# Kernel optimization log

Hardware: AMD Instinct MI355X
Metric: run time of the kernel (lower is better)

## Reference

```python
import jax, jax.numpy as jnp
import numpy as np

DIM = 32
HID = 128          # edge-MLP hidden width
N = 8192           # total nodes
E = 131072         # total edges
B = 64             # number of graphs
NUM_MP = 3
S2S_STEPS = 3


def setup_inputs() -> dict:
    key = jax.random.key(0)
    ks = jax.random.split(key, 24)
    g = lambda k, shape, s=0.05: jax.random.normal(k, shape, dtype=jnp.float32) * s

    inp = {
        "x": jax.random.normal(ks[0], (N, 1), dtype=jnp.float32),
        "edge_attr": jax.random.uniform(ks[1], (E, 2), dtype=jnp.float32),
        # params
        "lin0_w": g(ks[2], (1, DIM)), "lin0_b": g(ks[3], (DIM,)),
        "enn_w1": g(ks[4], (2, HID)), "enn_b1": g(ks[5], (HID,)),
        "enn_w2": g(ks[6], (HID, DIM * DIM)), "enn_b2": g(ks[7], (DIM * DIM,)),
        "root_w": g(ks[8], (DIM, DIM)), "conv_b": g(ks[9], (DIM,)),
        # GRU (gates ordered r,z,n as in torch)
        "gru_wih": g(ks[10], (DIM, 3 * DIM)), "gru_whh": g(ks[11], (DIM, 3 * DIM)),
        "gru_bih": g(ks[12], (3 * DIM,)), "gru_bhh": g(ks[13], (3 * DIM,)),
        # Set2Set LSTM: input 2*DIM, hidden DIM (gates ordered i,f,g,o as in torch)
        "s2s_wih": g(ks[14], (2 * DIM, 4 * DIM)), "s2s_whh": g(ks[15], (DIM, 4 * DIM)),
        "s2s_bih": g(ks[16], (4 * DIM,)), "s2s_bhh": g(ks[17], (4 * DIM,)),
        "lin1_w": g(ks[18], (2 * DIM, DIM)), "lin1_b": g(ks[19], (DIM,)),
        "lin2_w": g(ks[20], (DIM, 1)), "lin2_b": g(ks[21], (1,)),
        # int args
        "edge_index": jax.random.randint(ks[22], (2, E), 0, N, dtype=jnp.int32),
        "batch": jnp.sort(jax.random.randint(ks[23], (N,), 0, B, dtype=jnp.int32)),
    }
    return inp


def _forward(x, edge_attr, lin0_w, lin0_b, enn_w1, enn_b1, enn_w2, enn_b2,
             root_w, conv_b, gru_wih, gru_whh, gru_bih, gru_bhh,
             s2s_wih, s2s_whh, s2s_bih, s2s_bhh, lin1_w, lin1_b, lin2_w, lin2_b,
             edge_index, batch):
    src, dst = edge_index[0], edge_index[1]

    out = jax.nn.relu(x @ lin0_w + lin0_b)          # [N, DIM]
    h = out                                          # GRU hidden state

    # edge-conditioned weights (constant across MP layers -> hoisted)
    ew = jax.nn.relu(edge_attr @ enn_w1 + enn_b1) @ enn_w2 + enn_b2
    W = ew.reshape(E, DIM, DIM)                      # [E, in, out]

    deg = jnp.maximum(jax.ops.segment_sum(jnp.ones((E,), jnp.float32), dst,
                                          num_segments=N), 1.0)[:, None]

    for _ in range(NUM_MP):
        # NNConv: gather -> per-edge small matmul -> scatter-mean, + root + bias
        msg = jnp.einsum('ed,edo->eo', out[src], W)  # [E, DIM]
        agg = jax.ops.segment_sum(msg, dst, num_segments=N) / deg
        m = jax.nn.relu(agg + out @ root_w + conv_b)
        # GRU cell (single step)
        gi = m @ gru_wih + gru_bih
        gh = h @ gru_whh + gru_bhh
        ir, iz, in_ = jnp.split(gi, 3, axis=-1)
        hr, hz, hn = jnp.split(gh, 3, axis=-1)
        r = jax.nn.sigmoid(ir + hr)
        z = jax.nn.sigmoid(iz + hz)
        n = jnp.tanh(in_ + r * hn)
        h = (1.0 - z) * n + z * h
        out = h

    # Set2Set pooling
    qh = jnp.zeros((B, DIM), jnp.float32)
    qc = jnp.zeros((B, DIM), jnp.float32)
    q_star = jnp.zeros((B, 2 * DIM), jnp.float32)
    for _ in range(S2S_STEPS):
        gates = q_star @ s2s_wih + s2s_bih + qh @ s2s_whh + s2s_bhh
        i_, f_, g_, o_ = jnp.split(gates, 4, axis=-1)
        qc = jax.nn.sigmoid(f_) * qc + jax.nn.sigmoid(i_) * jnp.tanh(g_)
        qh = jax.nn.sigmoid(o_) * jnp.tanh(qc)       # [B, DIM]
        e = jnp.sum(out * qh[batch], axis=-1)        # [N] attention logits
        emax = jax.ops.segment_max(e, batch, num_segments=B)
        a = jnp.exp(e - emax[batch])
        a = a / jax.ops.segment_sum(a, batch, num_segments=B)[batch]
        r_read = jax.ops.segment_sum(a[:, None] * out, batch, num_segments=B)
        q_star = jnp.concatenate([qh, r_read], axis=-1)  # [B, 2*DIM]

    y = jax.nn.relu(q_star @ lin1_w + lin1_b) @ lin2_w + lin2_b
    return y.reshape(-1)                              # [B]


def reference(x, edge_attr, lin0_w, lin0_b, enn_w1, enn_b1, enn_w2, enn_b2,
              root_w, conv_b, gru_wih, gru_whh, gru_bih, gru_bhh,
              s2s_wih, s2s_whh, s2s_bih, s2s_bhh, lin1_w, lin1_b, lin2_w, lin2_b,
              edge_index, batch):
    return _forward(x, edge_attr, lin0_w, lin0_b, enn_w1, enn_b1, enn_w2, enn_b2,
                    root_w, conv_b, gru_wih, gru_whh, gru_bih, gru_bhh,
                    s2s_wih, s2s_whh, s2s_bih, s2s_bhh, lin1_w, lin1_b, lin2_w,
                    lin2_b, edge_index, batch)
```

## Files before the change

kernel.cpp:

```cpp
#include <hip/hip_runtime.h>

#define N_NODES 8192
#define N_EDGES 131072
#define NGRAPH  64
#define DIM     32
#define HID     128
#define KHALF   64
#define G_NODES 3
#define SROW    34

__device__ __forceinline__ float sigmoidf_(float x) { return 1.0f / (1.0f + expf(-x)); }

__global__ void prep1_kernel(const float* __restrict__ x, const float* __restrict__ w,
                             const float* __restrict__ b, float* __restrict__ out,
                             const int* __restrict__ dst, int* __restrict__ counts) {
  const int bb = blockIdx.x;
  if (bb < 1024) {
    int idx = bb * 256 + threadIdx.x;
    int n = idx >> 5, d = idx & 31;
    out[idx] = fmaxf(fmaf(x[n], w[d], b[d]), 0.0f);
  } else {
    int e = (bb - 1024) * 256 + threadIdx.x;
    atomicAdd(&counts[dst[e]], 1);
  }
}

__global__ void scan_kernel(const int* __restrict__ counts,
                            int* __restrict__ offsets,
                            float* __restrict__ deg_inv) {
  __shared__ int sm[1024];
  int t = threadIdx.x;
  int base = t * 8;
  int loc[8];
  int s = 0;
#pragma unroll
  for (int i = 0; i < 8; ++i) { loc[i] = s; s += counts[base + i]; }
  sm[t] = s;
  __syncthreads();
  for (int off = 1; off < 1024; off <<= 1) {
    int v = (t >= off) ? sm[t - off] : 0;
    __syncthreads();
    sm[t] += v;
    __syncthreads();
  }
  int excl = (t > 0) ? sm[t - 1] : 0;
#pragma unroll
  for (int i = 0; i < 8; ++i) {
    offsets[base + i] = excl + loc[i];
    int c = counts[base + i];
    deg_inv[base + i] = 1.0f / (float)(c > 0 ? c : 1);
  }
  if (t == 1023) offsets[N_NODES] = sm[1023];
}

__global__ void prep2_kernel(const int* __restrict__ ei, const float* __restrict__ ea,
                             const int* __restrict__ offsets, int* __restrict__ cursor,
                             int* __restrict__ csr_src, float2* __restrict__ csr_ea,
                             const int* __restrict__ batch, int* __restrict__ gstart) {
  const int bb = blockIdx.x;
  if (bb < 512) {
    int e = bb * 256 + threadIdx.x;
    int d = ei[N_EDGES + e];
    int pos = atomicAdd(&cursor[d], 1);
    int slot = offsets[d] + pos;
    csr_src[slot] = ei[e];
    csr_ea[slot] = make_float2(ea[2 * e], ea[2 * e + 1]);
  } else {
    int n = (bb - 512) * 256 + threadIdx.x;
    int b = batch[n];
    if (n == 0) {
      for (int g = 0; g <= b; ++g) gstart[g] = 0;
    } else {
      int bp = batch[n - 1];
      for (int g = bp + 1; g <= b; ++g) gstart[g] = n;
    }
    if (n == N_NODES - 1) {
      for (int g = b + 1; g <= NGRAPH; ++g) gstart[g] = N_NODES;
    }
  }
}

__global__ __launch_bounds__(256, 4) void mp_half_kernel(
    const float* __restrict__ out_cur, const int* __restrict__ offsets,
    const int* __restrict__ csr_src, const float2* __restrict__ csr_ea,
    const float* __restrict__ w1, const float* __restrict__ b1,
    const float* __restrict__ w2, float* __restrict__ partial,
    float* __restrict__ O) {
  constexpr int C = 16;
  __shared__ float smem[G_NODES * KHALF * SROW + C * KHALF + C * DIM];
  float* S = smem;
  float* hidb = smem + G_NODES * KHALF * SROW;
  float* osrcb = hidb + C * KHALF;
  float* red = smem;
  __shared__ int offs[G_NODES + 1];

  const int t = threadIdx.x;
  const int bb = blockIdx.x;
  const int khalf = bb & 1;
  const int node0 = (bb >> 1) * G_NODES;

  if (t <= G_NODES) offs[t] = offsets[min(node0 + t, N_NODES)];

  const int kg = t >> 4, dg = t & 15;
  const int k0 = kg * 4, d0 = dg * 2;
  const int ec = t >> 4, sub = t & 15;

  float acc[G_NODES][4][2];
#pragma unroll
  for (int g = 0; g < G_NODES; ++g)
#pragma unroll
    for (int i = 0; i < 4; ++i) { acc[g][i][0] = 0.0f; acc[g][i][1] = 0.0f; }
  float oacc[G_NODES] = {0.0f, 0.0f, 0.0f};
  __syncthreads();

#pragma unroll
  for (int g = 0; g < G_NODES; ++g) {
    const int base = offs[g], end = offs[g + 1];
    for (int c0 = base; c0 < end; c0 += C) {
      const int cnt = min(C, end - c0);
      __syncthreads();
      if (ec < cnt) {
        const int slot = c0 + ec;
        const float2 eav = csr_ea[slot];
        const int sidx = csr_src[slot];
#pragma unroll
        for (int i = 0; i < 4; ++i) {
          const int kl = sub * 4 + i;
          const int kgl = khalf * KHALF + kl;
          hidb[ec * KHALF + kl] =
              fmaxf(fmaf(eav.y, w1[HID + kgl], fmaf(eav.x, w1[kgl], b1[kgl])), 0.0f);
        }
        *(float2*)(osrcb + ec * DIM + sub * 2) =
            *(const float2*)(out_cur + sidx * DIM + sub * 2);
      }
      __syncthreads();
      for (int e = 0; e < cnt; ++e) {
        const float4 hv = *(const float4*)(hidb + e * KHALF + k0);
        const float2 ov = *(const float2*)(osrcb + e * DIM + d0);
        acc[g][0][0] = fmaf(hv.x, ov.x, acc[g][0][0]);
        acc[g][0][1] = fmaf(hv.x, ov.y, acc[g][0][1]);
        acc[g][1][0] = fmaf(hv.y, ov.x, acc[g][1][0]);
        acc[g][1][1] = fmaf(hv.y, ov.y, acc[g][1][1]);
        acc[g][2][0] = fmaf(hv.z, ov.x, acc[g][2][0]);
        acc[g][2][1] = fmaf(hv.z, ov.y, acc[g][2][1]);
        acc[g][3][0] = fmaf(hv.w, ov.x, acc[g][3][0]);
        acc[g][3][1] = fmaf(hv.w, ov.y, acc[g][3][1]);
        if (khalf == 0 && t < DIM) oacc[g] += osrcb[e * DIM + t];
      }
    }
  }
#pragma unroll
  for (int g = 0; g < G_NODES; ++g) {
    float* Sg = S + g * KHALF * SROW;
#pragma unroll
    for (int i = 0; i < 4; ++i)
      *(float2*)(Sg + (k0 + i) * SROW + d0) = make_float2(acc[g][i][0], acc[g][i][1]);
  }
  if (khalf == 0 && t < DIM) {
#pragma unroll
    for (int g = 0; g < G_NODES; ++g) {
      const int node = node0 + g;
      if (node < N_NODES) O[node * DIM + t] = oacc[g];
    }
  }
  __syncthreads();

  {
    const int ks = t >> 4;
    const int dvh = (t >> 3) & 1;
    const int og = t & 7;
    float a4[G_NODES][4];
#pragma unroll
    for (int g = 0; g < G_NODES; ++g)
#pragma unroll
      for (int r = 0; r < 4; ++r) a4[g][r] = 0.0f;
#pragma unroll
    for (int i = 0; i < 4; ++i) {
      const int kl = ks * 4 + i;
      const float* w2k = w2 + (size_t)(khalf * KHALF + kl) * (DIM * DIM);
#pragma unroll
      for (int dvi = 0; dvi < 4; ++dvi) {
        const int dv = dvh * 4 + dvi;
#pragma unroll
        for (int r = 0; r < 4; ++r) {
          const int d = dv * 4 + r;
          const float4 wv = *(const float4*)(w2k + d * DIM + og * 4);
#pragma unroll
          for (int g = 0; g < G_NODES; ++g) {
            const float sv = S[g * KHALF * SROW + kl * SROW + d];
            a4[g][0] = fmaf(sv, wv.x, a4[g][0]);
            a4[g][1] = fmaf(sv, wv.y, a4[g][1]);
            a4[g][2] = fmaf(sv, wv.z, a4[g][2]);
            a4[g][3] = fmaf(sv, wv.w, a4[g][3]);
          }
        }
      }
    }
    __syncthreads();
#pragma unroll
    for (int g = 0; g < G_NODES; ++g)
#pragma unroll
      for (int r = 0; r < 4; ++r) red[(g * 4 + r) * 256 + t] = a4[g][r];
  }
  __syncthreads();
  if (t < G_NODES * DIM) {
    const int g = t >> 5, o = t & 31;
    const int og = o >> 2, r = o & 3;
    const float* rp = red + (g * 4 + r) * 256 + og;
    float sum = 0.0f;
#pragma unroll
    for (int j = 0; j < 32; ++j) sum += rp[j * 8];
    const int node = node0 + g;
    if (node < N_NODES)
      partial[(size_t)khalf * N_NODES * DIM + node * DIM + o] = sum;
  }
}

__global__ __launch_bounds__(256) void epilogue_kernel(
    const float* __restrict__ partial, const float* __restrict__ O,
    const float* __restrict__ out_cur, const float* __restrict__ b2,
    const float* __restrict__ deg_inv, const float* __restrict__ root_w,
    const float* __restrict__ conv_b, const float* __restrict__ gwih,
    const float* __restrict__ gwhh, const float* __restrict__ gbih,
    const float* __restrict__ gbhh, float* __restrict__ out_nxt) {
  __shared__ float hb[256], ob[256], mb[256], b2s[1024];
  const int t = threadIdx.x;
  const int node0 = blockIdx.x * 8;
  hb[t] = out_cur[node0 * DIM + t];
  ob[t] = O[node0 * DIM + t];
#pragma unroll
  for (int i = 0; i < 4; ++i) b2s[i * 256 + t] = b2[i * 256 + t];
  __syncthreads();
  const int g = t >> 5, o = t & 31;
  const int node = node0 + g;
  float agg = partial[node * DIM + o] +
              partial[(size_t)N_NODES * DIM + node * DIM + o];
#pragma unroll
  for (int d = 0; d < DIM; ++d) agg = fmaf(ob[g * DIM + d], b2s[d * DIM + o], agg);
  agg *= deg_inv[node];
  float rt = conv_b[o];
#pragma unroll
  for (int d = 0; d < DIM; ++d) rt = fmaf(hb[g * DIM + d], root_w[d * DIM + o], rt);
  mb[t] = fmaxf(agg + rt, 0.0f);
  __syncthreads();
  float gi[3], gh[3];
#pragma unroll
  for (int jj = 0; jj < 3; ++jj) {
    float si = gbih[jj * DIM + o], sh = gbhh[jj * DIM + o];
#pragma unroll
    for (int d = 0; d < DIM; ++d) {
      si = fmaf(mb[g * DIM + d], gwih[d * 3 * DIM + jj * DIM + o], si);
      sh = fmaf(hb[g * DIM + d], gwhh[d * 3 * DIM + jj * DIM + o], sh);
    }
    gi[jj] = si;
    gh[jj] = sh;
  }
  const float r = sigmoidf_(gi[0] + gh[0]);
  const float z = sigmoidf_(gi[1] + gh[1]);
  const float nn = tanhf(fmaf(r, gh[2], gi[2]));
  out_nxt[node * DIM + o] = (1.0f - z) * nn + z * hb[t];
}

__global__ __launch_bounds__(256) void s2s_kernel(
    const float* __restrict__ outf, const int* __restrict__ gstart,
    const float* __restrict__ wih, const float* __restrict__ whh,
    const float* __restrict__ bih, const float* __restrict__ bhh,
    const float* __restrict__ l1w, const float* __restrict__ l1b,
    const float* __restrict__ l2w, const float* __restrict__ l2b,
    float* __restrict__ y) {
  __shared__ float qh[DIM], qc[DIM], qstar[2 * DIM], gates[4 * DIM];
  __shared__ float wsum[4], wmax[4], wr[4][DIM];
  const int b = blockIdx.x, t = threadIdx.x;
  const int gs = gstart[b], ge = gstart[b + 1];
  const int w = t >> 6, lane = t & 63;
  if (t < DIM) { qh[t] = 0.0f; qc[t] = 0.0f; }
  if (t < 2 * DIM) qstar[t] = 0.0f;
  __syncthreads();
  for (int step = 0; step < 3; ++step) {
    if (t < 4 * DIM) {
      float gv = bih[t] + bhh[t];
      for (int i = 0; i < 2 * DIM; ++i) gv = fmaf(qstar[i], wih[i * 4 * DIM + t], gv);
      for (int i = 0; i < DIM; ++i) gv = fmaf(qh[i], whh[i * 4 * DIM + t], gv);
      gates[t] = gv;
    }
    __syncthreads();
    if (t < DIM) {
      const float ig = sigmoidf_(gates[t]);
      const float fg = sigmoidf_(gates[DIM + t]);
      const float gg = tanhf(gates[2 * DIM + t]);
      const float og = sigmoidf_(gates[3 * DIM + t]);
      const float c = fmaf(fg, qc[t], ig * gg);
      qc[t] = c;
      qh[t] = og * tanhf(c);
    }
    __syncthreads();
    float lmax = -INFINITY;
    for (int n = gs + t; n < ge; n += 256) {
      const float* orow = outf + n * DIM;
      float e = 0.0f;
#pragma unroll
      for (int d = 0; d < DIM; ++d) e = fmaf(orow[d], qh[d], e);
      lmax = fmaxf(lmax, e);
    }
#pragma unroll
    for (int off = 32; off > 0; off >>= 1) lmax = fmaxf(lmax, __shfl_xor(lmax, off));
    if (lane == 0) wmax[w] = lmax;
    __syncthreads();
    const float gmax = fmaxf(fmaxf(wmax[0], wmax[1]), fmaxf(wmax[2], wmax[3]));
    float rl[DIM];
#pragma unroll
    for (int d = 0; d < DIM; ++d) rl[d] = 0.0f;
    float lsum = 0.0f;
    for (int n = gs + t; n < ge; n += 256) {
      const float* orow = outf + n * DIM;
      float e = 0.0f;
#pragma unroll
      for (int d = 0; d < DIM; ++d) e = fmaf(orow[d], qh[d], e);
      const float a = expf(e - gmax);
      lsum += a;
#pragma unroll
      for (int d = 0; d < DIM; ++d) rl[d] = fmaf(a, orow[d], rl[d]);
    }
#pragma unroll
    for (int off = 32; off > 0; off >>= 1) {
      lsum += __shfl_xor(lsum, off);
#pragma unroll
      for (int d = 0; d < DIM; ++d) rl[d] += __shfl_xor(rl[d], off);
    }
    __syncthreads();
    if (lane == 0) {
      wsum[w] = lsum;
#pragma unroll
      for (int d = 0; d < DIM; ++d) wr[w][d] = rl[d];
    }
    __syncthreads();
    if (t < DIM) {
      const float stot = wsum[0] + wsum[1] + wsum[2] + wsum[3];
      const float rv = wr[0][t] + wr[1][t] + wr[2][t] + wr[3][t];
      qstar[t] = qh[t];
      qstar[DIM + t] = (stot > 0.0f) ? rv / stot : 0.0f;
    }
    __syncthreads();
  }
  if (t < DIM) {
    float u = l1b[t];
    for (int i = 0; i < 2 * DIM; ++i) u = fmaf(qstar[i], l1w[i * DIM + t], u);
    u = fmaxf(u, 0.0f);
    float v = u * l2w[t];
#pragma unroll
    for (int off = 16; off > 0; off >>= 1) v += __shfl_xor(v, off);
    if (t == 0) y[b] = v + l2b[0];
  }
}

extern "C" void kernel_launch(void* const* d_in, const int* in_sizes, int n_in,
                              void* d_out, int out_size, void* d_ws, size_t ws_size,
                              hipStream_t stream) {
  const float* x        = (const float*)d_in[0];
  const float* ea       = (const float*)d_in[1];
  const float* lin0_w   = (const float*)d_in[2];
  const float* lin0_b   = (const float*)d_in[3];
  const float* enn_w1   = (const float*)d_in[4];
  const float* enn_b1   = (const float*)d_in[5];
  const float* enn_w2   = (const float*)d_in[6];
  const float* enn_b2   = (const float*)d_in[7];
  const float* root_w   = (const float*)d_in[8];
  const float* conv_b   = (const float*)d_in[9];
  const float* gru_wih  = (const float*)d_in[10];
  const float* gru_whh  = (const float*)d_in[11];
  const float* gru_bih  = (const float*)d_in[12];
  const float* gru_bhh  = (const float*)d_in[13];
  const float* s2s_wih  = (const float*)d_in[14];
  const float* s2s_whh  = (const float*)d_in[15];
  const float* s2s_bih  = (const float*)d_in[16];
  const float* s2s_bhh  = (const float*)d_in[17];
  const float* lin1_w   = (const float*)d_in[18];
  const float* lin1_b   = (const float*)d_in[19];
  const float* lin2_w   = (const float*)d_in[20];
  const float* lin2_b   = (const float*)d_in[21];
  const int*   ei       = (const int*)d_in[22];
  const int*   batch    = (const int*)d_in[23];
  float* y = (float*)d_out;

  char* p = (char*)d_ws;
  auto alloc = [&](size_t bytes) -> void* {
    void* r = (void*)p;
    p += (bytes + 255) & ~(size_t)255;
    return r;
  };
  float*  out_a   = (float*)alloc(N_NODES * DIM * 4);
  float*  out_b   = (float*)alloc(N_NODES * DIM * 4);
  int*    counts  = (int*)alloc(N_NODES * 4);
  int*    offsets = (int*)alloc((N_NODES + 1) * 4);
  int*    cursor  = (int*)alloc(N_NODES * 4);
  int*    csr_src = (int*)alloc(N_EDGES * 4);
  float2* csr_ea  = (float2*)alloc(N_EDGES * 8);
  float*  deg_inv = (float*)alloc(N_NODES * 4);
  int*    gstart  = (int*)alloc((NGRAPH + 1) * 4);
  float*  Obuf    = (float*)alloc((size_t)N_NODES * DIM * 4);
  float*  partial = (float*)alloc((size_t)2 * N_NODES * DIM * 4);
  (void)ws_size; (void)n_in; (void)in_sizes; (void)out_size;

  hipMemsetAsync(counts, 0, N_NODES * 4, stream);
  hipMemsetAsync(cursor, 0, N_NODES * 4, stream);

  prep1_kernel<<<1024 + 512, 256, 0, stream>>>(x, lin0_w, lin0_b, out_a,
                                               ei + N_EDGES, counts);
  scan_kernel<<<1, 1024, 0, stream>>>(counts, offsets, deg_inv);
  prep2_kernel<<<512 + 32, 256, 0, stream>>>(ei, ea, offsets, cursor, csr_src,
                                             csr_ea, batch, gstart);

  const int ngroups = (N_NODES + G_NODES - 1) / G_NODES;
  const float* cur = out_a;
  float* nxt = out_b;
  for (int layer = 0; layer < 3; ++layer) {
    mp_half_kernel<<<ngroups * 2, 256, 0, stream>>>(
        cur, offsets, csr_src, csr_ea, enn_w1, enn_b1, enn_w2, partial, Obuf);
    epilogue_kernel<<<N_NODES / 8, 256, 0, stream>>>(
        partial, Obuf, cur, enn_b2, deg_inv, root_w, conv_b,
        gru_wih, gru_whh, gru_bih, gru_bhh, nxt);
    const float* tmp = cur; cur = nxt; nxt = (float*)tmp;
  }

  s2s_kernel<<<NGRAPH, 256, 0, stream>>>(cur, gstart, s2s_wih, s2s_whh, s2s_bih,
                                         s2s_bhh, lin1_w, lin1_b, lin2_w, lin2_b, y);
}
```

Measured before the change: 455.1 us.

## Alias edge staging buffers onto S, swizzle S layout, hoist enn layer-1 weights

The edge staging buffers (hidden activations and source features) now share shared memory with the S accumulator tile, which shrinks LDS per block and raises the occupancy hint from 4 to 5 blocks. The edge chunk size doubles to 32 and the per-edge layer-1 weights are hoisted into registers. Each thread now stages 8 hidden values and a float4 of source features. The S tile uses a padded row of 36 with an XOR-like rotation so the second stage can read float4s, and the reduction stride is padded to 257 to avoid bank conflicts. Costs are more registers per thread and an extra barrier before S is written over the aliased staging area.

Measured after the change: 424.2 us. 6.8% less time.

```diff
diff --git a/kernel.cpp b/kernel.cpp
--- a/kernel.cpp
+++ b/kernel.cpp
@@ -7,7 +7,7 @@
 #define HID     128
 #define KHALF   64
 #define G_NODES 3
-#define SROW    34
+#define SROW    36
 
 __device__ __forceinline__ float sigmoidf_(float x) { return 1.0f / (1.0f + expf(-x)); }
 
@@ -80,17 +80,17 @@
   }
 }
 
-__global__ __launch_bounds__(256, 4) void mp_half_kernel(
+__global__ __launch_bounds__(256, 5) void mp_half_kernel(
     const float* __restrict__ out_cur, const int* __restrict__ offsets,
     const int* __restrict__ csr_src, const float2* __restrict__ csr_ea,
     const float* __restrict__ w1, const float* __restrict__ b1,
     const float* __restrict__ w2, float* __restrict__ partial,
     float* __restrict__ O) {
-  constexpr int C = 16;
-  __shared__ float smem[G_NODES * KHALF * SROW + C * KHALF + C * DIM];
+  constexpr int C = 32;
+  __shared__ float smem[G_NODES * KHALF * SROW];
   float* S = smem;
-  float* hidb = smem + G_NODES * KHALF * SROW;
-  float* osrcb = hidb + C * KHALF;
+  float* hidb = smem;
+  float* osrcb = smem + C * KHALF;
   float* red = smem;
   __shared__ int offs[G_NODES + 1];
 
@@ -103,7 +103,16 @@
 
   const int kg = t >> 4, dg = t & 15;
   const int k0 = kg * 4, d0 = dg * 2;
-  const int ec = t >> 4, sub = t & 15;
+  const int ec = t >> 3, sub = t & 7;
+
+  float w1x[8], w1y[8], b1v[8];
+#pragma unroll
+  for (int i = 0; i < 8; ++i) {
+    const int kgl = khalf * KHALF + sub * 8 + i;
+    w1x[i] = w1[kgl];
+    w1y[i] = w1[HID + kgl];
+    b1v[i] = b1[kgl];
+  }
 
   float acc[G_NODES][4][2];
 #pragma unroll
@@ -123,38 +132,45 @@
         const int slot = c0 + ec;
         const float2 eav = csr_ea[slot];
         const int sidx = csr_src[slot];
-#pragma unroll
-        for (int i = 0; i < 4; ++i) {
-          const int kl = sub * 4 + i;
-          const int kgl = khalf * KHALF + kl;
-          hidb[ec * KHALF + kl] =
-              fmaxf(fmaf(eav.y, w1[HID + kgl], fmaf(eav.x, w1[kgl], b1[kgl])), 0.0f);
-        }
-        *(float2*)(osrcb + ec * DIM + sub * 2) =
-            *(const float2*)(out_cur + sidx * DIM + sub * 2);
+        float hv[8];
+#pragma unroll
+        for (int i = 0; i < 8; ++i)
+          hv[i] = fmaxf(fmaf(eav.y, w1y[i], fmaf(eav.x, w1x[i], b1v[i])), 0.0f);
+        *(float4*)(hidb + ec * KHALF + sub * 8) =
+            make_float4(hv[0], hv[1], hv[2], hv[3]);
+        *(float4*)(hidb + ec * KHALF + sub * 8 + 4) =
+            make_float4(hv[4], hv[5], hv[6], hv[7]);
+        *(float4*)(osrcb + ec * DIM + sub * 4) =
+            *(const float4*)(out_cur + sidx * DIM + sub * 4);
       }
       __syncthreads();
       for (int e = 0; e < cnt; ++e) {
-        const float4 hv = *(const float4*)(hidb + e * KHALF + k0);
+        const float4 hvv = *(const float4*)(hidb + e * KHALF + k0);
         const float2 ov = *(const float2*)(osrcb + e * DIM + d0);
-        acc[g][0][0] = fmaf(hv.x, ov.x, acc[g][0][0]);
-        acc[g][0][1] = fmaf(hv.x, ov.y, acc[g][0][1]);
-        acc[g][1][0] = fmaf(hv.y, ov.x, acc[g][1][0]);
-        acc[g][1][1] = fmaf(hv.y, ov.y, acc[g][1][1]);
-        acc[g][2][0] = fmaf(hv.z, ov.x, acc[g][2][0]);
-        acc[g][2][1] = fmaf(hv.z, ov.y, acc[g][2][1]);
-        acc[g][3][0] = fmaf(hv.w, ov.x, acc[g][3][0]);
-        acc[g][3][1] = fmaf(hv.w, ov.y, acc[g][3][1]);
+        acc[g][0][0] = fmaf(hvv.x, ov.x, acc[g][0][0]);
+        acc[g][0][1] = fmaf(hvv.x, ov.y, acc[g][0][1]);
+        acc[g][1][0] = fmaf(hvv.y, ov.x, acc[g][1][0]);
+        acc[g][1][1] = fmaf(hvv.y, ov.y, acc[g][1][1]);
+        acc[g][2][0] = fmaf(hvv.z, ov.x, acc[g][2][0]);
+        acc[g][2][1] = fmaf(hvv.z, ov.y, acc[g][2][1]);
+        acc[g][3][0] = fmaf(hvv.w, ov.x, acc[g][3][0]);
+        acc[g][3][1] = fmaf(hvv.w, ov.y, acc[g][3][1]);
         if (khalf == 0 && t < DIM) oacc[g] += osrcb[e * DIM + t];
       }
     }
   }
-#pragma unroll
-  for (int g = 0; g < G_NODES; ++g) {
-    float* Sg = S + g * KHALF * SROW;
-#pragma unroll
-    for (int i = 0; i < 4; ++i)
-      *(float2*)(Sg + (k0 + i) * SROW + d0) = make_float2(acc[g][i][0], acc[g][i][1]);
+  __syncthreads();
+
+  {
+    const int shift = (kg & 3) * 8;
+    const int dd = (d0 + shift) & 31;
+#pragma unroll
+    for (int g = 0; g < G_NODES; ++g) {
+      float* Sg = S + g * KHALF * SROW;
+#pragma unroll
+      for (int i = 0; i < 4; ++i)
+        *(float2*)(Sg + (k0 + i) * SROW + dd) = make_float2(acc[g][i][0], acc[g][i][1]);
+    }
   }
   if (khalf == 0 && t < DIM) {
 #pragma unroll
@@ -169,6 +185,7 @@
     const int ks = t >> 4;
     const int dvh = (t >> 3) & 1;
     const int og = t & 7;
+    const int shift = (ks & 3) * 8;
     float a4[G_NODES][4];
 #pragma unroll
     for (int g = 0; g < G_NODES; ++g)
@@ -179,20 +196,30 @@
       const int kl = ks * 4 + i;
       const float* w2k = w2 + (size_t)(khalf * KHALF + kl) * (DIM * DIM);
 #pragma unroll
-      for (int dvi = 0; dvi < 4; ++dvi) {
-        const int dv = dvh * 4 + dvi;
+      for (int q = 0; q < 4; ++q) {
+        const int dbase = dvh * 16 + q * 4;
+        const int dq = (dbase + shift) & 31;
+        const float4 sv0 = *(const float4*)(S + 0 * KHALF * SROW + kl * SROW + dq);
+        const float4 sv1 = *(const float4*)(S + 1 * KHALF * SROW + kl * SROW + dq);
+        const float4 sv2 = *(const float4*)(S + 2 * KHALF * SROW + kl * SROW + dq);
+        const float* s0 = (const float*)&sv0;
+        const float* s1 = (const float*)&sv1;
+        const float* s2 = (const float*)&sv2;
 #pragma unroll
         for (int r = 0; r < 4; ++r) {
-          const int d = dv * 4 + r;
-          const float4 wv = *(const float4*)(w2k + d * DIM + og * 4);
-#pragma unroll
-          for (int g = 0; g < G_NODES; ++g) {
-            const float sv = S[g * KHALF * SROW + kl * SROW + d];
-            a4[g][0] = fmaf(sv, wv.x, a4[g][0]);
-            a4[g][1] = fmaf(sv, wv.y, a4[g][1]);
-            a4[g][2] = fmaf(sv, wv.z, a4[g][2]);
-            a4[g][3] = fmaf(sv, wv.w, a4[g][3]);
-          }
+          const float4 wv = *(const float4*)(w2k + (dbase + r) * DIM + og * 4);
+          a4[0][0] = fmaf(s0[r], wv.x, a4[0][0]);
+          a4[0][1] = fmaf(s0[r], wv.y, a4[0][1]);
+          a4[0][2] = fmaf(s0[r], wv.z, a4[0][2]);
+          a4[0][3] = fmaf(s0[r], wv.w, a4[0][3]);
+          a4[1][0] = fmaf(s1[r], wv.x, a4[1][0]);
+          a4[1][1] = fmaf(s1[r], wv.y, a4[1][1]);
+          a4[1][2] = fmaf(s1[r], wv.z, a4[1][2]);
+          a4[1][3] = fmaf(s1[r], wv.w, a4[1][3]);
+          a4[2][0] = fmaf(s2[r], wv.x, a4[2][0]);
+          a4[2][1] = fmaf(s2[r], wv.y, a4[2][1]);
+          a4[2][2] = fmaf(s2[r], wv.z, a4[2][2]);
+          a4[2][3] = fmaf(s2[r], wv.w, a4[2][3]);
         }
       }
     }
@@ -200,13 +227,13 @@
 #pragma unroll
     for (int g = 0; g < G_NODES; ++g)
 #pragma unroll
-      for (int r = 0; r < 4; ++r) red[(g * 4 + r) * 256 + t] = a4[g][r];
+      for (int r = 0; r < 4; ++r) red[(g * 4 + r) * 257 + t] = a4[g][r];
   }
   __syncthreads();
   if (t < G_NODES * DIM) {
     const int g = t >> 5, o = t & 31;
     const int og = o >> 2, r = o & 3;
-    const float* rp = red + (g * 4 + r) * 256 + og;
+    const float* rp = red + (g * 4 + r) * 257 + og;
     float sum = 0.0f;
 #pragma unroll
     for (int j = 0; j < 32; ++j) sum += rp[j * 8];
```
